# Kernel optimization log

Hardware: AMD Instinct MI355X
Metric: run time of the kernel (lower is better)

## Reference

```python
import jax, jax.numpy as jnp
import numpy as np

FILTER_WIDTH = 23
NSIG = 9.0
RATIO = 4.0
SUB_LOW_RATIO = 1.0
PCT = 3.0  # normalization_percentile_threshold


def _gaussian_kernel_2d(ksize, sigma):
    # matches cv2.getGaussianKernel for sigma > 0: normalized 1D gaussian, outer product
    i = np.arange(ksize, dtype=np.float64) - (ksize - 1) / 2.0
    k1 = np.exp(-(i ** 2) / (2.0 * sigma ** 2))
    k1 /= k1.sum()
    k2 = np.outer(k1, k1)
    return k2.astype(np.float32)


def setup_inputs() -> dict:
    key = jax.random.key(0)
    k1, k2 = jax.random.split(key)
    x = jax.random.normal(k1, (16, 3, 512, 512), dtype=jnp.float32)
    mask = jax.random.uniform(k2, (16, 1, 512, 512), dtype=jnp.float32)
    kernel = jnp.asarray(_gaussian_kernel_2d(FILTER_WIDTH, NSIG))[None, None]  # [1,1,23,23]
    return {"x": x, "mask": mask, "kernel": kernel}


def reference(x, mask, kernel):
    N, C, H, W = x.shape
    pad = FILTER_WIDTH // 2  # 11

    # --- median padding (torch.median = lower median -> sorted index (n-1)//2) ---
    flat = x.reshape(N, C, H * W)
    med = jnp.sort(flat, axis=-1)[:, :, (H * W - 1) // 2] + 0.2  # [N,C]
    med = med[:, :, None, None]
    xp = mask * x + (1.0 - mask) * med  # [N,C,H,W]

    # --- Gaussian low-pass: replication pad + depthwise conv (same kernel per channel) ---
    xpad = jnp.pad(xp, ((0, 0), (0, 0), (pad, pad), (pad, pad)), mode="edge")
    k = jnp.broadcast_to(kernel, (C, 1, FILTER_WIDTH, FILTER_WIDTH))
    gauss = jax.lax.conv_general_dilated(
        xpad, k, window_strides=(1, 1), padding="VALID", feature_group_count=C
    )  # [N,C,H,W]

    res = RATIO * (xp - SUB_LOW_RATIO * gauss)

    # --- per-(n,c) percentile normalization on 1/256-quantized copy ---
    temp = jnp.trunc(res * 256.0) / 256.0  # torch .int() truncates toward zero
    tflat = temp.reshape(N, C, H * W)
    lo = jnp.percentile(tflat, PCT, axis=-1)[:, :, None, None]
    hi = jnp.percentile(tflat, 100.0 - PCT, axis=-1)[:, :, None, None]
    res = (res - lo) / (hi - lo)

    # sub_mask=True
    return res * mask
```

## Files before the change

### kernel.cpp

```cpp
#include <hip/hip_runtime.h>

#define HW 262144
#define WID 512
#define PLANES 48
#define NCH 3
#define PAD 11
#define FW 23
#define XS 92
#define HS 64

__global__ __launch_bounds__(256) void hist1_kernel(const float* __restrict__ x,
                                                    int* __restrict__ ghist1) {
  __shared__ int h[8192];
  const int p = blockIdx.x, s = blockIdx.y, tid = threadIdx.x;
  for (int i = tid; i < 8192; i += 256) h[i] = 0;
  __syncthreads();
  const float4* xv = (const float4*)(x + (size_t)p * HW + (size_t)s * (HW / 16));
#define H1(c) { int b = (int)(((c) + 8.0f) * 512.0f); b = min(max(b, 0), 8191); atomicAdd(&h[b], 1); }
  for (int i = tid; i < HW / 16 / 4; i += 256) {
    float4 v = xv[i];
    H1(v.x); H1(v.y); H1(v.z); H1(v.w);
  }
#undef H1
  __syncthreads();
  int* gh = ghist1 + p * 8192;
  const int st = (s * 512) & 8191;
  for (int k = tid; k < 8192; k += 256) {
    int i = (k + st) & 8191;
    int c = h[i];
    if (c) atomicAdd(&gh[i], c);
  }
}

__global__ __launch_bounds__(256) void scan_med_kernel(const int* __restrict__ ghist1,
                                                       float* __restrict__ med,
                                                       const float* __restrict__ kern,
                                                       float* __restrict__ k1g) {
  __shared__ int incl[256];
  __shared__ int s_chunk, s_base;
  const int p = blockIdx.x, t = threadIdx.x;
  if (p == 0 && t < FW) k1g[t] = kern[t * FW + PAD] / sqrtf(kern[PAD * FW + PAD]);
  const int* gh = ghist1 + p * 8192;
  int mysum = 0;
#pragma unroll
  for (int j = 0; j < 32; ++j) mysum += gh[t * 32 + j];
  incl[t] = mysum;
  __syncthreads();
  for (int off = 1; off < 256; off <<= 1) {
    int v = (t >= off) ? incl[t - off] : 0;
    __syncthreads();
    incl[t] += v;
    __syncthreads();
  }
  const int rank = 131072;
  {
    int excl = incl[t] - mysum;
    if (excl < rank && rank <= incl[t]) { s_chunk = t; s_base = rank - excl; }
  }
  __syncthreads();
  if (t < 64) {
    const int c = s_chunk, base = s_base;
    int cnt = (t < 32) ? gh[c * 32 + t] : 0;
    int pfx = cnt;
#pragma unroll
    for (int off = 1; off < 32; off <<= 1) {
      int u = __shfl_up(pfx, off, 64);
      if (t >= off) pfx += u;
    }
    unsigned long long m = __ballot(t < 32 && pfx >= base);
    int bin = c * 32 + (__ffsll((long long)m) - 1);
    if (t == 0) med[p] = -8.0f + ((float)bin + 0.5f) * 0.001953125f + 0.2f;
  }
}

__global__ __launch_bounds__(256) void conv_kernel(const float* __restrict__ x,
                                                   const float* __restrict__ mask,
                                                   const float* __restrict__ k1g,
                                                   const float* __restrict__ med,
                                                   float* __restrict__ res) {
  __shared__ float xs[86 * XS];
  __shared__ float hs[86 * HS];
  const int z = blockIdx.z;
  const int n = z / NCH;
  const int tbx = blockIdx.x, tby = blockIdx.y;
  const int tid = threadIdx.x;

  float k1[FW];
#pragma unroll
  for (int t = 0; t < FW; ++t) k1[t] = k1g[t];

  const float m_med = med[z];
  const int gr0 = tby * 64 - PAD;
  const int gc0 = tbx * 64 - PAD;
  const float* xb = x + (size_t)z * HW;
  const float* mb = mask + (size_t)n * HW;
  for (int i = tid; i < 86 * 86; i += 256) {
    int r = i / 86, c = i - r * 86;
    int gr = min(max(gr0 + r, 0), WID - 1);
    int gc = min(max(gc0 + c, 0), WID - 1);
    int g = gr * WID + gc;
    float xv = xb[g], mv = mb[g];
    xs[r * XS + c] = fmaf(mv, xv - m_med, m_med);
  }
  __syncthreads();

  for (int g = tid; g < 86 * 8; g += 256) {
    int r = g >> 3, c0 = (g & 7) << 3;
    const float* row = &xs[r * XS + c0];
    float w[32];
#pragma unroll
    for (int q = 0; q < 8; ++q) *(float4*)&w[q * 4] = *(const float4*)(row + q * 4);
    float a[8];
#pragma unroll
    for (int j = 0; j < 8; ++j) a[j] = 0.f;
#pragma unroll
    for (int t = 0; t < FW; ++t) {
      float k = k1[t];
#pragma unroll
      for (int j = 0; j < 8; ++j) a[j] = fmaf(k, w[t + j], a[j]);
    }
    *(float4*)&hs[r * HS + c0] = make_float4(a[0], a[1], a[2], a[3]);
    *(float4*)&hs[r * HS + c0 + 4] = make_float4(a[4], a[5], a[6], a[7]);
  }
  __syncthreads();

  const int ct = (tid & 15) << 2;
  const int rt = (tid >> 4) << 2;
  float4 acc[4];
#pragma unroll
  for (int j = 0; j < 4; ++j) acc[j] = make_float4(0.f, 0.f, 0.f, 0.f);
#pragma unroll
  for (int tp = 0; tp < 26; ++tp) {
    float4 v = *(const float4*)&hs[(rt + tp) * HS + ct];
    const int jlo = (tp - 22 > 0) ? (tp - 22) : 0;
    const int jhi = (tp < 3) ? tp : 3;
#pragma unroll
    for (int j = jlo; j <= jhi; ++j) {
      float k = k1[tp - j];
      acc[j].x = fmaf(k, v.x, acc[j].x);
      acc[j].y = fmaf(k, v.y, acc[j].y);
      acc[j].z = fmaf(k, v.z, acc[j].z);
      acc[j].w = fmaf(k, v.w, acc[j].w);
    }
  }

  float* rb = res + (size_t)z * HW + (size_t)(tby * 64) * WID + tbx * 64;
#pragma unroll
  for (int j = 0; j < 4; ++j) {
    const float* xr = &xs[(rt + j + PAD) * XS + ct];
    float4 A = *(const float4*)(xr + 8);
    float4 B = *(const float4*)(xr + 12);
    float4 o;
    o.x = 4.0f * (A.w - acc[j].x);
    o.y = 4.0f * (B.x - acc[j].y);
    o.z = 4.0f * (B.y - acc[j].z);
    o.w = 4.0f * (B.z - acc[j].w);
    *(float4*)&rb[(size_t)(rt + j) * WID + ct] = o;
  }
}

__global__ __launch_bounds__(256) void hist_kernel(const float* __restrict__ res,
                                                   int* __restrict__ ghist) {
  __shared__ int h[8192];
  const int p = blockIdx.x, s = blockIdx.y, tid = threadIdx.x;
  for (int i = tid; i < 8192; i += 256) h[i] = 0;
  __syncthreads();
  const float4* rv = (const float4*)(res + (size_t)p * HW + (size_t)s * (HW / 16));
#define HADD(c) { int b = (int)((c) * 256.0f) + 4096; b = min(max(b, 0), 8191); atomicAdd(&h[b], 1); }
  for (int i = tid; i < HW / 16 / 4; i += 256) {
    float4 v = rv[i];
    HADD(v.x); HADD(v.y); HADD(v.z); HADD(v.w);
  }
#undef HADD
  __syncthreads();
  int* gh = ghist + p * 8192;
  const int st = (s * 512) & 8191;
  for (int k = tid; k < 8192; k += 256) {
    int i = (k + st) & 8191;
    int c = h[i];
    if (c) atomicAdd(&gh[i], c);
  }
}

__global__ __launch_bounds__(256) void pct_kernel(const int* __restrict__ ghist,
                                                  float* __restrict__ lo_out,
                                                  float* __restrict__ inv_out) {
  __shared__ int incl[256];
  __shared__ int s_chunk, s_base;
  __shared__ float s_v[4];
  const int p = blockIdx.x, t = threadIdx.x;
  const int* gh = ghist + p * 8192;
  int mysum = 0;
#pragma unroll
  for (int j = 0; j < 32; ++j) mysum += gh[t * 32 + j];
  incl[t] = mysum;
  __syncthreads();
  for (int off = 1; off < 256; off <<= 1) {
    int v = (t >= off) ? incl[t - off] : 0;
    __syncthreads();
    incl[t] += v;
    __syncthreads();
  }
  const int ranks[4] = {7865, 7866, 254279, 254280};
#pragma unroll
  for (int r = 0; r < 4; ++r) {
    const int rank = ranks[r];
    int excl = incl[t] - mysum;
    if (excl < rank && rank <= incl[t]) { s_chunk = t; s_base = rank - excl; }
    __syncthreads();
    if (t < 64) {
      const int c = s_chunk, base = s_base;
      int cnt = (t < 32) ? gh[c * 32 + t] : 0;
      int pfx = cnt;
#pragma unroll
      for (int off = 1; off < 32; off <<= 1) {
        int u = __shfl_up(pfx, off, 64);
        if (t >= off) pfx += u;
      }
      unsigned long long m = __ballot(t < 32 && pfx >= base);
      int bin = c * 32 + (__ffsll((long long)m) - 1);
      if (t == 0) s_v[r] = (float)(bin - 4096) * 0.00390625f;
    }
    __syncthreads();
  }
  if (t == 0) {
    const double fl = 0.29, fh = 0.71;
    double lov = (double)s_v[0] + fl * ((double)s_v[1] - (double)s_v[0]);
    double hiv = (double)s_v[2] + fh * ((double)s_v[3] - (double)s_v[2]);
    lo_out[p] = (float)lov;
    inv_out[p] = (float)(1.0 / (hiv - lov));
  }
}

__global__ __launch_bounds__(256) void final_kernel(float* __restrict__ res,
                                                    const float* __restrict__ mask,
                                                    const float* __restrict__ lo,
                                                    const float* __restrict__ inv) {
  const int i = blockIdx.x * 256 + threadIdx.x;
  const int e = i << 2;
  const int z = e >> 18;
  const int n = z / NCH;
  const int hw = e & (HW - 1);
  float4 r = ((const float4*)res)[i];
  float4 m = *(const float4*)(mask + (size_t)n * HW + hw);
  const float l = lo[z];
  const float iv = inv[z];
  float4 o;
  o.x = (r.x - l) * iv * m.x;
  o.y = (r.y - l) * iv * m.y;
  o.z = (r.z - l) * iv * m.z;
  o.w = (r.w - l) * iv * m.w;
  ((float4*)res)[i] = o;
}

extern "C" void kernel_launch(void* const* d_in, const int* in_sizes, int n_in,
                              void* d_out, int out_size, void* d_ws, size_t ws_size,
                              hipStream_t stream) {
  (void)in_sizes; (void)n_in; (void)out_size; (void)ws_size;
  const float* x = (const float*)d_in[0];
  const float* mask = (const float*)d_in[1];
  const float* kern = (const float*)d_in[2];
  float* out = (float*)d_out;

  int* hist = (int*)d_ws;
  int* ghist1 = hist + PLANES * 8192;
  float* med = (float*)(ghist1 + PLANES * 8192);
  float* lo = med + PLANES;
  float* inv = lo + PLANES;
  float* k1g = inv + PLANES;

  hipMemsetAsync(hist, 0, (size_t)PLANES * (8192 + 8192) * sizeof(int), stream);
  hist1_kernel<<<dim3(PLANES, 16), 256, 0, stream>>>(x, ghist1);
  scan_med_kernel<<<PLANES, 256, 0, stream>>>(ghist1, med, kern, k1g);
  conv_kernel<<<dim3(8, 8, PLANES), 256, 0, stream>>>(x, mask, k1g, med, out);
  hist_kernel<<<dim3(PLANES, 16), 256, 0, stream>>>(out, hist);
  pct_kernel<<<PLANES, 256, 0, stream>>>(hist, lo, inv);
  final_kernel<<<(HW * PLANES / 4 + 255) / 256, 256, 0, stream>>>(out, mask, lo, inv);
}
```

Measured before the change: 214.2 us.

## Fuse result histogram into conv kernel, use bf16 shared tiles and taller tiles

Builds the per-plane histogram of the residual inside the convolution kernel from register values, so the separate hist kernel and its re-read of the output are gone. The shared-memory tiles now hold bf16 values, which halves LDS footprint, and each block handles a 64x128 tile so less halo is recomputed. Storing intermediates in bf16 lowers precision, which can shift the quantized percentile bins and the final output.

```diff
diff --git a/kernel.cpp b/kernel.cpp
--- a/kernel.cpp
+++ b/kernel.cpp
@@ -6,8 +6,25 @@
 #define NCH 3
 #define PAD 11
 #define FW 23
-#define XS 92
-#define HS 64
+#define TW 64
+#define TH 128
+#define XR 150
+#define XC 88
+#define HC 64
+
+__device__ __forceinline__ unsigned pack_bf16(float a, float b) {
+  unsigned ua = (__float_as_uint(a) + 0x8000u) >> 16;
+  unsigned ub = (__float_as_uint(b) + 0x8000u) & 0xFFFF0000u;
+  return ub | ua;
+}
+__device__ __forceinline__ float lo_bf16(unsigned u) { return __uint_as_float(u << 16); }
+__device__ __forceinline__ float hi_bf16(unsigned u) { return __uint_as_float(u & 0xFFFF0000u); }
+__device__ __forceinline__ void unpack8(uint4 v, float* f) {
+  f[0] = lo_bf16(v.x); f[1] = hi_bf16(v.x);
+  f[2] = lo_bf16(v.y); f[3] = hi_bf16(v.y);
+  f[4] = lo_bf16(v.z); f[5] = hi_bf16(v.z);
+  f[6] = lo_bf16(v.w); f[7] = hi_bf16(v.w);
+}
 
 __global__ __launch_bounds__(256) void hist1_kernel(const float* __restrict__ x,
                                                     int* __restrict__ ghist1) {
@@ -77,9 +94,11 @@
                                                    const float* __restrict__ mask,
                                                    const float* __restrict__ k1g,
                                                    const float* __restrict__ med,
-                                                   float* __restrict__ res) {
-  __shared__ float xs[86 * XS];
-  __shared__ float hs[86 * HS];
+                                                   float* __restrict__ res,
+                                                   int* __restrict__ ghist) {
+  __shared__ unsigned smem[11400];
+  unsigned short* xs = (unsigned short*)smem;
+  unsigned short* hs = (unsigned short*)smem + XR * XC;
   const int z = blockIdx.z;
   const int n = z / NCH;
   const int tbx = blockIdx.x, tby = blockIdx.y;
@@ -90,26 +109,31 @@
   for (int t = 0; t < FW; ++t) k1[t] = k1g[t];
 
   const float m_med = med[z];
-  const int gr0 = tby * 64 - PAD;
-  const int gc0 = tbx * 64 - PAD;
+  const int gr0 = tby * TH - PAD;
+  const int gc0 = tbx * TW - PAD;
   const float* xb = x + (size_t)z * HW;
   const float* mb = mask + (size_t)n * HW;
-  for (int i = tid; i < 86 * 86; i += 256) {
-    int r = i / 86, c = i - r * 86;
+
+  for (int i = tid; i < XR * (XC / 2); i += 256) {
+    int r = i / (XC / 2), pc = i - r * (XC / 2);
     int gr = min(max(gr0 + r, 0), WID - 1);
-    int gc = min(max(gc0 + c, 0), WID - 1);
-    int g = gr * WID + gc;
-    float xv = xb[g], mv = mb[g];
-    xs[r * XS + c] = fmaf(mv, xv - m_med, m_med);
-  }
-  __syncthreads();
-
-  for (int g = tid; g < 86 * 8; g += 256) {
+    int gc = min(max(gc0 + 2 * pc, 0), WID - 1);
+    int gc2 = min(max(gc0 + 2 * pc + 1, 0), WID - 1);
+    float a = fmaf(mb[gr * WID + gc], xb[gr * WID + gc] - m_med, m_med);
+    float b = fmaf(mb[gr * WID + gc2], xb[gr * WID + gc2] - m_med, m_med);
+    ((unsigned*)xs)[r * (XC / 2) + pc] = pack_bf16(a, b);
+  }
+  __syncthreads();
+
+  for (int g = tid; g < XR * 8; g += 256) {
     int r = g >> 3, c0 = (g & 7) << 3;
-    const float* row = &xs[r * XS + c0];
+    const unsigned* row = (const unsigned*)&xs[r * XC] + (c0 >> 1);
+    uint4 A = *(const uint4*)row;
+    uint4 B = *(const uint4*)(row + 4);
+    uint4 C = *(const uint4*)(row + 8);
+    uint4 D = *(const uint4*)(row + 12);
     float w[32];
-#pragma unroll
-    for (int q = 0; q < 8; ++q) *(float4*)&w[q * 4] = *(const float4*)(row + q * 4);
+    unpack8(A, w); unpack8(B, w + 8); unpack8(C, w + 16); unpack8(D, w + 24);
     float a[8];
 #pragma unroll
     for (int j = 0; j < 8; ++j) a[j] = 0.f;
@@ -119,65 +143,73 @@
 #pragma unroll
       for (int j = 0; j < 8; ++j) a[j] = fmaf(k, w[t + j], a[j]);
     }
-    *(float4*)&hs[r * HS + c0] = make_float4(a[0], a[1], a[2], a[3]);
-    *(float4*)&hs[r * HS + c0 + 4] = make_float4(a[4], a[5], a[6], a[7]);
-  }
-  __syncthreads();
-
-  const int ct = (tid & 15) << 2;
-  const int rt = (tid >> 4) << 2;
-  float4 acc[4];
-#pragma unroll
-  for (int j = 0; j < 4; ++j) acc[j] = make_float4(0.f, 0.f, 0.f, 0.f);
-#pragma unroll
-  for (int tp = 0; tp < 26; ++tp) {
-    float4 v = *(const float4*)&hs[(rt + tp) * HS + ct];
+    uint4 o;
+    o.x = pack_bf16(a[0], a[1]); o.y = pack_bf16(a[2], a[3]);
+    o.z = pack_bf16(a[4], a[5]); o.w = pack_bf16(a[6], a[7]);
+    *(uint4*)((unsigned*)&hs[r * HC] + (c0 >> 1)) = o;
+  }
+  __syncthreads();
+
+  const int ct = (tid & 7) << 3;
+  const int rt = (tid >> 3) << 2;
+  float acc[4][8];
+#pragma unroll
+  for (int j = 0; j < 4; ++j)
+#pragma unroll
+    for (int q = 0; q < 8; ++q) acc[j][q] = 0.f;
+#pragma unroll
+  for (int tp = 0; tp <= 25; ++tp) {
+    uint4 v = *(const uint4*)((const unsigned*)&hs[(rt + tp) * HC] + (ct >> 1));
+    float f[8];
+    unpack8(v, f);
     const int jlo = (tp - 22 > 0) ? (tp - 22) : 0;
     const int jhi = (tp < 3) ? tp : 3;
 #pragma unroll
     for (int j = jlo; j <= jhi; ++j) {
       float k = k1[tp - j];
-      acc[j].x = fmaf(k, v.x, acc[j].x);
-      acc[j].y = fmaf(k, v.y, acc[j].y);
-      acc[j].z = fmaf(k, v.z, acc[j].z);
-      acc[j].w = fmaf(k, v.w, acc[j].w);
-    }
-  }
-
-  float* rb = res + (size_t)z * HW + (size_t)(tby * 64) * WID + tbx * 64;
+#pragma unroll
+      for (int q = 0; q < 8; ++q) acc[j][q] = fmaf(k, f[q], acc[j][q]);
+    }
+  }
+
+  float* rb = res + (size_t)z * HW + (size_t)(tby * TH + rt) * WID + (tbx * TW + ct);
 #pragma unroll
   for (int j = 0; j < 4; ++j) {
-    const float* xr = &xs[(rt + j + PAD) * XS + ct];
-    float4 A = *(const float4*)(xr + 8);
-    float4 B = *(const float4*)(xr + 12);
-    float4 o;
-    o.x = 4.0f * (A.w - acc[j].x);
-    o.y = 4.0f * (B.x - acc[j].y);
-    o.z = 4.0f * (B.y - acc[j].z);
-    o.w = 4.0f * (B.z - acc[j].w);
-    *(float4*)&rb[(size_t)(rt + j) * WID + ct] = o;
-  }
-}
-
-__global__ __launch_bounds__(256) void hist_kernel(const float* __restrict__ res,
-                                                   int* __restrict__ ghist) {
-  __shared__ int h[8192];
-  const int p = blockIdx.x, s = blockIdx.y, tid = threadIdx.x;
-  for (int i = tid; i < 8192; i += 256) h[i] = 0;
-  __syncthreads();
-  const float4* rv = (const float4*)(res + (size_t)p * HW + (size_t)s * (HW / 16));
-#define HADD(c) { int b = (int)((c) * 256.0f) + 4096; b = min(max(b, 0), 8191); atomicAdd(&h[b], 1); }
-  for (int i = tid; i < HW / 16 / 4; i += 256) {
-    float4 v = rv[i];
-    HADD(v.x); HADD(v.y); HADD(v.z); HADD(v.w);
-  }
-#undef HADD
-  __syncthreads();
-  int* gh = ghist + p * 8192;
-  const int st = (s * 512) & 8191;
+    const unsigned* xr = (const unsigned*)&xs[(rt + j + PAD) * XC] + ((ct + 8) >> 1);
+    uint4 A = *(const uint4*)xr;
+    uint4 B = *(const uint4*)(xr + 4);
+    float xp[8];
+    xp[0] = hi_bf16(A.y); xp[1] = lo_bf16(A.z); xp[2] = hi_bf16(A.z); xp[3] = lo_bf16(A.w);
+    xp[4] = hi_bf16(A.w); xp[5] = lo_bf16(B.x); xp[6] = hi_bf16(B.x); xp[7] = lo_bf16(B.y);
+    float4 o0, o1;
+    o0.x = 4.0f * (xp[0] - acc[j][0]); o0.y = 4.0f * (xp[1] - acc[j][1]);
+    o0.z = 4.0f * (xp[2] - acc[j][2]); o0.w = 4.0f * (xp[3] - acc[j][3]);
+    o1.x = 4.0f * (xp[4] - acc[j][4]); o1.y = 4.0f * (xp[5] - acc[j][5]);
+    o1.z = 4.0f * (xp[6] - acc[j][6]); o1.w = 4.0f * (xp[7] - acc[j][7]);
+    *(float4*)&rb[(size_t)j * WID] = o0;
+    *(float4*)&rb[(size_t)j * WID + 4] = o1;
+    acc[j][0] = o0.x; acc[j][1] = o0.y; acc[j][2] = o0.z; acc[j][3] = o0.w;
+    acc[j][4] = o1.x; acc[j][5] = o1.y; acc[j][6] = o1.z; acc[j][7] = o1.w;
+  }
+
+  __syncthreads();
+  int* hh = (int*)smem;
+  for (int i = tid; i < 8192; i += 256) hh[i] = 0;
+  __syncthreads();
+#pragma unroll
+  for (int j = 0; j < 4; ++j)
+#pragma unroll
+    for (int q = 0; q < 8; ++q) {
+      int b = (int)(acc[j][q] * 256.0f) + 4096;
+      b = min(max(b, 0), 8191);
+      atomicAdd(&hh[b], 1);
+    }
+  __syncthreads();
+  int* gh = ghist + z * 8192;
+  const int st = ((tbx * 4 + tby) * 256) & 8191;
   for (int k = tid; k < 8192; k += 256) {
     int i = (k + st) & 8191;
-    int c = h[i];
+    int c = hh[i];
     if (c) atomicAdd(&gh[i], c);
   }
 }
@@ -262,18 +294,17 @@
   const float* kern = (const float*)d_in[2];
   float* out = (float*)d_out;
 
-  int* hist = (int*)d_ws;
-  int* ghist1 = hist + PLANES * 8192;
+  int* ghist = (int*)d_ws;
+  int* ghist1 = ghist + PLANES * 8192;
   float* med = (float*)(ghist1 + PLANES * 8192);
   float* lo = med + PLANES;
   float* inv = lo + PLANES;
   float* k1g = inv + PLANES;
 
-  hipMemsetAsync(hist, 0, (size_t)PLANES * (8192 + 8192) * sizeof(int), stream);
+  hipMemsetAsync(ghist, 0, (size_t)PLANES * (8192 + 8192) * sizeof(int), stream);
   hist1_kernel<<<dim3(PLANES, 16), 256, 0, stream>>>(x, ghist1);
   scan_med_kernel<<<PLANES, 256, 0, stream>>>(ghist1, med, kern, k1g);
-  conv_kernel<<<dim3(8, 8, PLANES), 256, 0, stream>>>(x, mask, k1g, med, out);
-  hist_kernel<<<dim3(PLANES, 16), 256, 0, stream>>>(out, hist);
-  pct_kernel<<<PLANES, 256, 0, stream>>>(hist, lo, inv);
+  conv_kernel<<<dim3(8, 4, PLANES), 256, 0, stream>>>(x, mask, k1g, med, out, ghist);
+  pct_kernel<<<PLANES, 256, 0, stream>>>(ghist, lo, inv);
   final_kernel<<<(HW * PLANES / 4 + 255) / 256, 256, 0, stream>>>(out, mask, lo, inv);
 }
```

Measured after the change: 220.0 us. +2.7%, slower.
